# Optimization experiments

Measured on AMD Instinct MI355X. Metric: run time of the kernel, lower is better.

The kernel has to match this reference:

```python
import jax, jax.numpy as jnp
import numpy as np

B, S, D = 4, 2048, 2048
H, HD = 16, 128
ROPE_THETA = 10000.0


def rotate_half(x):
    half = x.shape[-1] // 2
    return jnp.concatenate([-x[..., half:], x[..., :half]], axis=-1)


def setup_inputs() -> dict:
    key = jax.random.key(0)
    ks = jax.random.split(key, 5)
    scale = 1.0 / np.sqrt(D)
    x = jax.random.normal(ks[0], (B, S, D), dtype=jnp.float32)
    wq = jax.random.normal(ks[1], (D, H * HD), dtype=jnp.float32) * scale
    wk = jax.random.normal(ks[2], (D, H * HD), dtype=jnp.float32) * scale
    wv = jax.random.normal(ks[3], (D, H * HD), dtype=jnp.float32) * scale
    wo = jax.random.normal(ks[4], (H * HD, D), dtype=jnp.float32) * scale
    # RoPE frequencies: freqs_cis real/imag parts, shape [S, HD//2]
    inv_freq = 1.0 / (ROPE_THETA ** (np.arange(0, HD, 2, dtype=np.float32) / HD))
    t = np.arange(S, dtype=np.float32)
    freqs = np.outer(t, inv_freq)  # [S, HD//2]
    cos = jnp.asarray(np.cos(freqs), dtype=jnp.float32)
    sin = jnp.asarray(np.sin(freqs), dtype=jnp.float32)
    return {"x": x, "wq": wq, "wk": wk, "wv": wv, "wo": wo, "cos": cos, "sin": sin}


def reference(x, wq, wk, wv, wo, cos, sin):
    batch, seq_len, _ = x.shape
    # QKV projections (no bias), reshape to [b, h, s, d]
    q = (x @ wq).reshape(batch, seq_len, H, HD).transpose(0, 2, 1, 3)
    k = (x @ wk).reshape(batch, seq_len, H, HD).transpose(0, 2, 1, 3)
    v = (x @ wv).reshape(batch, seq_len, H, HD)  # [b, s, h, d]
    # RoPE (half-split / rotate_half convention)
    cos_full = jnp.concatenate([cos, cos], axis=-1)[None, None, :seq_len, :]
    sin_full = jnp.concatenate([sin, sin], axis=-1)[None, None, :seq_len, :]
    q = q * cos_full + rotate_half(q) * sin_full
    k = k * cos_full + rotate_half(k) * sin_full
    # Scaled dot-product attention with causal mask
    logits = jnp.einsum('bhqd,bhkd->bhqk', q, k) / jnp.sqrt(jnp.float32(HD))
    causal = jnp.tril(jnp.ones((seq_len, seq_len), dtype=bool))
    logits = jnp.where(causal[None, None, :, :], logits, -1e10)
    weights = jax.nn.softmax(logits, axis=-1)
    out = jnp.einsum('bhqk,bkhd->bqhd', weights, v)
    out = out.reshape(batch, seq_len, H * HD)
    return out @ wo
```

## Files before the change

kernel.cpp:

```cpp
#include <hip/hip_runtime.h>
#include <cstdint>
#include <cstddef>

typedef unsigned short u16;
using bf16x8  = __attribute__((ext_vector_type(8))) short;
using floatx4 = __attribute__((ext_vector_type(4))) float;

__device__ __forceinline__ u16 f2bf(float f) {
    union { float f; unsigned u; } v; v.f = f;
    unsigned r = v.u + 0x7fffu + ((v.u >> 16) & 1u);
    return (u16)(r >> 16);
}
__device__ __forceinline__ float bf2f(u16 h) {
    union { unsigned u; float f; } v; v.u = ((unsigned)h) << 16; return v.f;
}
__device__ __forceinline__ floatx4 mfma16(bf16x8 a, bf16x8 b, floatx4 c) {
    return __builtin_amdgcn_mfma_f32_16x16x32_bf16(a, b, c, 0, 0, 0);
}
using gptr_t = const __attribute__((address_space(1))) unsigned int*;
using lptr_t = __attribute__((address_space(3))) unsigned int*;
__device__ __forceinline__ void lds16(const void* g, void* l) {
    __builtin_amdgcn_global_load_lds((gptr_t)g, (lptr_t)l, 16, 0, 0);
}
typedef __attribute__((address_space(3))) const u16* lds_cp;
__device__ __forceinline__ bf16x8 dsr128(const u16* p) {
    bf16x8 r;
    asm volatile("ds_read_b128 %0, %1" : "=v"(r) : "v"((lds_cp)p));
    return r;
}

#define ATT_SCALE 0.1275758218522532f

__global__ __launch_bounds__(256) void cvt_x(const float* __restrict__ x, u16* __restrict__ xb) {
    size_t i = ((size_t)blockIdx.x * 256 + threadIdx.x) * 4;
    float4 v = *(const float4*)&x[i];
    ushort4 r; r.x = f2bf(v.x); r.y = f2bf(v.y); r.z = f2bf(v.z); r.w = f2bf(v.w);
    *(ushort4*)&xb[i] = r;
}

__global__ __launch_bounds__(256) void transpose_wall(const float* __restrict__ wq, const float* __restrict__ wk,
                                                      const float* __restrict__ wv, const float* __restrict__ wo,
                                                      u16* __restrict__ wqkvb, u16* __restrict__ wob) {
    __shared__ float t[64][65];
    const int z = blockIdx.z;
    const float* in = (z == 0) ? wq : (z == 1) ? wk : (z == 2) ? wv : wo;
    u16* out = (z < 3) ? (wqkvb + (size_t)z * 2048 * 2048) : wob;
    int k0 = blockIdx.x * 64, n0 = blockIdx.y * 64;
    int tx = threadIdx.x, ty = threadIdx.y;
#pragma unroll
    for (int i = 0; i < 16; ++i) {
        int r = i * 4 + ty;
        t[r][tx] = in[(size_t)(k0 + r) * 2048 + n0 + tx];
    }
    __syncthreads();
#pragma unroll
    for (int i = 0; i < 16; ++i) {
        int r = i * 4 + ty;
        out[(size_t)(n0 + r) * 2048 + k0 + tx] = f2bf(t[tx][r]);
    }
}

template <int MODE>
__global__ __launch_bounds__(512, 2) void gemm_bt(const u16* __restrict__ A, const u16* __restrict__ B,
                                                  u16* __restrict__ Qo, u16* __restrict__ Ko, u16* __restrict__ Vt,
                                                  float* __restrict__ Co) {
    __shared__ __align__(16) u16 sA[2][16384];
    __shared__ __align__(16) u16 sB[2][16384];

    const int nbx = (MODE == 0) ? 24 : 8;
    const int bid = blockIdx.x;
    const int q8 = (int)gridDim.x >> 3;
    const int wg = (bid & 7) * q8 + (bid >> 3);
    const int bx = wg % nbx, by = wg / nbx;
    const int m0 = by << 8, n0 = bx << 8;

    const int tid = threadIdx.x;
    const int w = tid >> 6, lane = tid & 63;
    const int wm = w >> 2, wn = w & 3;
    const int m16 = lane & 15, q4 = lane >> 4;
    const int lr = lane >> 3;
    const int lc8 = (lane & 7) ^ lr;

    const u16* Ag = A + (size_t)(m0 + w * 16 + lr) * 2048 + lc8 * 8;
    const u16* Bg = B + (size_t)(n0 + w * 16 + lr) * 2048 + lc8 * 8;

    const int swz0 = ((q4 ^ (m16 & 7)) << 3);
    const int swz1 = (((4 + q4) ^ (m16 & 7)) << 3);

    floatx4 acc[8][4];
#pragma unroll
    for (int r = 0; r < 8; ++r)
#pragma unroll
        for (int c = 0; c < 4; ++c) acc[r][c] = (floatx4)0.0f;
    bf16x8 af[4][2];
    bf16x8 bf[4][2];

#define STAGE_A(b, h, t) do { \
    lds16(Ag + (size_t)((h) * 128) * 2048 + (t) * 64,     &sA[b][(h) * 8192 + w * 1024]);       \
    lds16(Ag + (size_t)((h) * 128 + 8) * 2048 + (t) * 64, &sA[b][(h) * 8192 + w * 1024 + 512]); \
} while (0)
#define STAGE_B(b, h, t) do { \
    lds16(Bg + (size_t)((h) * 128) * 2048 + (t) * 64,     &sB[b][(h) * 8192 + w * 1024]);       \
    lds16(Bg + (size_t)((h) * 128 + 8) * 2048 + (t) * 64, &sB[b][(h) * 8192 + w * 1024 + 512]); \
} while (0)
#define BAR() __builtin_amdgcn_s_barrier()
#define WAITL0() do { asm volatile("s_waitcnt lgkmcnt(0)" ::: "memory"); __builtin_amdgcn_sched_barrier(0); } while (0)
#define WAITL8() asm volatile("s_waitcnt lgkmcnt(8)" ::: "memory")
#define LDA_(cur, mq) do { _Pragma("unroll") for (int fr = 0; fr < 4; ++fr) { \
    const u16* p = &sA[cur][(wm * 128 + (mq) * 64 + fr * 16 + m16) * 64];      \
    af[fr][0] = dsr128(&p[swz0]);                                              \
    af[fr][1] = dsr128(&p[swz1]); } } while (0)
#define LDB_(cur, nq) do { _Pragma("unroll") for (int c = 0; c < 2; ++c) {     \
    const u16* p = &sB[cur][(wn * 64 + ((nq) * 2 + c) * 16 + m16) * 64];       \
    bf[(nq) * 2 + c][0] = dsr128(&p[swz0]);                                    \
    bf[(nq) * 2 + c][1] = dsr128(&p[swz1]); } } while (0)
#define MM_(mq, nq) do { _Pragma("unroll") for (int kk = 0; kk < 2; ++kk)      \
    _Pragma("unroll") for (int fr = 0; fr < 4; ++fr)                           \
    _Pragma("unroll") for (int c = 0; c < 2; ++c)                              \
        acc[(mq) * 4 + fr][(nq) * 2 + c] =                                     \
            mfma16(af[fr][kk], bf[(nq) * 2 + c][kk], acc[(mq) * 4 + fr][(nq) * 2 + c]); } while (0)

    const int NT = 32;

    STAGE_B(0, 0, 0); STAGE_B(0, 1, 0);
    STAGE_A(0, 0, 0); STAGE_A(0, 1, 0);
    STAGE_B(1, 0, 1); STAGE_B(1, 1, 1);
    asm volatile("s_waitcnt vmcnt(4)" ::: "memory");
    __builtin_amdgcn_s_barrier();

#pragma unroll 2
    for (int t = 0; t < NT; ++t) {
        const int cur = t & 1;
        LDB_(cur, 0);
        LDA_(cur, 0);
        if (t + 1 < NT) STAGE_A(cur ^ 1, 0, t + 1);
        WAITL8();
        BAR();
        WAITL0();
        __builtin_amdgcn_s_setprio(1); MM_(0, 0); __builtin_amdgcn_s_setprio(0);
        BAR();
        LDB_(cur, 1);
        if (t + 1 < NT) STAGE_A(cur ^ 1, 1, t + 1);
        BAR();
        WAITL0();
        __builtin_amdgcn_s_setprio(1); MM_(0, 1); __builtin_amdgcn_s_setprio(0);
        BAR();
        LDA_(cur, 1);
        if (t + 2 < NT) STAGE_B(cur, 0, t + 2);
        BAR();
        WAITL0();
        __builtin_amdgcn_s_setprio(1); MM_(1, 1); __builtin_amdgcn_s_setprio(0);
        BAR();
        if (t + 2 < NT) STAGE_B(cur, 1, t + 2);
        BAR();
        __builtin_amdgcn_s_setprio(1); MM_(1, 0); __builtin_amdgcn_s_setprio(0);
        if (t + 2 < NT)      { asm volatile("s_waitcnt vmcnt(4)" ::: "memory"); }
        else if (t + 1 < NT) { asm volatile("s_waitcnt vmcnt(0)" ::: "memory"); }
        BAR();
    }

#undef STAGE_A
#undef STAGE_B
#undef BAR
#undef WAITL0
#undef WAITL8
#undef LDA_
#undef LDB_
#undef MM_

    if (MODE == 0) {
        const int which = n0 >> 11;
        if (which < 2) {
            u16* dst = (which == 0) ? Qo : Ko;
#pragma unroll
            for (int fr = 0; fr < 8; ++fr) {
                const int mb = m0 + wm * 128 + fr * 16 + q4 * 4;
#pragma unroll
                for (int c = 0; c < 4; ++c) {
                    const int n = n0 + wn * 64 + c * 16 + m16;
                    const int h = (n >> 7) & 15, d = n & 127;
#pragma unroll
                    for (int i = 0; i < 4; ++i) {
                        const int mm = mb + i;
                        const int b = mm >> 11, s = mm & 2047;
                        dst[((size_t)((b * 16 + h) * 2048 + s) << 7) + d] = f2bf(acc[fr][c][i]);
                    }
                }
            }
        } else {
#pragma unroll
            for (int fr = 0; fr < 8; ++fr) {
                const int mb = m0 + wm * 128 + fr * 16 + q4 * 4;
                const int b = mb >> 11, s = mb & 2047;
#pragma unroll
                for (int c = 0; c < 4; ++c) {
                    const int n = n0 + wn * 64 + c * 16 + m16;
                    const int h = (n >> 7) & 15, d = n & 127;
                    ushort4 pk;
                    pk.x = f2bf(acc[fr][c][0]); pk.y = f2bf(acc[fr][c][1]);
                    pk.z = f2bf(acc[fr][c][2]); pk.w = f2bf(acc[fr][c][3]);
                    *(ushort4*)&Vt[((size_t)((b * 16 + h) * 128 + d)) * 2048 + s] = pk;
                }
            }
        }
    } else {
#pragma unroll
        for (int fr = 0; fr < 8; ++fr) {
            const int mb = m0 + wm * 128 + fr * 16 + q4 * 4;
#pragma unroll
            for (int c = 0; c < 4; ++c) {
                const int n = n0 + wn * 64 + c * 16 + m16;
#pragma unroll
                for (int i = 0; i < 4; ++i)
                    Co[(size_t)(mb + i) * 2048 + n] = acc[fr][c][i];
            }
        }
    }
}

__global__ __launch_bounds__(256) void rope_qk(u16* __restrict__ Q, u16* __restrict__ K,
                                               const float* __restrict__ cosb, const float* __restrict__ sinb) {
    int t = blockIdx.x * 256 + threadIdx.x;
    int d4 = (t & 15) * 4;
    int row = t >> 4;
    int s = row & 2047;
    float4 cs = *(const float4*)&cosb[s * 64 + d4];
    float4 sn = *(const float4*)&sinb[s * 64 + d4];
    size_t base = (size_t)row * 128;
    ushort4 qlo = *(ushort4*)&Q[base + d4];
    ushort4 qhi = *(ushort4*)&Q[base + 64 + d4];
    ushort4 klo = *(ushort4*)&K[base + d4];
    ushort4 khi = *(ushort4*)&K[base + 64 + d4];
    float ql[4] = {bf2f(qlo.x), bf2f(qlo.y), bf2f(qlo.z), bf2f(qlo.w)};
    float qh[4] = {bf2f(qhi.x), bf2f(qhi.y), bf2f(qhi.z), bf2f(qhi.w)};
    float kl[4] = {bf2f(klo.x), bf2f(klo.y), bf2f(klo.z), bf2f(klo.w)};
    float kh[4] = {bf2f(khi.x), bf2f(khi.y), bf2f(khi.z), bf2f(khi.w)};
    float c[4] = {cs.x, cs.y, cs.z, cs.w};
    float n[4] = {sn.x, sn.y, sn.z, sn.w};
    ushort4 o0, o1, o2, o3;
    u16* p0 = &o0.x; u16* p1 = &o1.x; u16* p2 = &o2.x; u16* p3 = &o3.x;
#pragma unroll
    for (int i = 0; i < 4; ++i) {
        p0[i] = f2bf((ql[i] * c[i] - qh[i] * n[i]) * ATT_SCALE);
        p1[i] = f2bf((qh[i] * c[i] + ql[i] * n[i]) * ATT_SCALE);
        p2[i] = f2bf(kl[i] * c[i] - kh[i] * n[i]);
        p3[i] = f2bf(kh[i] * c[i] + kl[i] * n[i]);
    }
    *(ushort4*)&Q[base + d4]      = o0;
    *(ushort4*)&Q[base + 64 + d4] = o1;
    *(ushort4*)&K[base + d4]      = o2;
    *(ushort4*)&K[base + 64 + d4] = o3;
}

__global__ __launch_bounds__(512) void attn_kernel(const u16* __restrict__ Q, const u16* __restrict__ K,
                                                   const u16* __restrict__ VT, u16* __restrict__ AO) {
    __shared__ __align__(16) u16 ks[64 * 136];
    __shared__ __align__(16) u16 vts[128 * 72];
    __shared__ __align__(16) u16 ps[256 * 72];
    static const int iqmap[8] = {7, 6, 5, 4, 0, 1, 2, 3};
    const int bx = blockIdx.x;
    const int iq = iqmap[bx >> 6];
    const int bh = bx & 63;
    const int b = bh >> 4, h = bh & 15;
    const u16* Qg = Q  + (size_t)bh * (2048 * 128);
    const u16* Kg = K  + (size_t)bh * (2048 * 128);
    const u16* Vg = VT + (size_t)bh * (128 * 2048);
    const int tid = threadIdx.x, w = tid >> 6, lane = tid & 63;
    const int m16 = lane & 15, q4 = lane >> 4;
    const int jn = 4 * iq + 4;

    const int qrow = iq * 256 + w * 32;
    bf16x8 qf[2][4];
#pragma unroll
    for (int rm = 0; rm < 2; ++rm)
#pragma unroll
        for (int kk = 0; kk < 4; ++kk)
            qf[rm][kk] = *(const bf16x8*)&Qg[(size_t)(qrow + rm * 16 + m16) * 128 + kk * 32 + q4 * 8];

    floatx4 o[2][8];
#pragma unroll
    for (int rm = 0; rm < 2; ++rm)
#pragma unroll
        for (int c = 0; c < 8; ++c) o[rm][c] = (floatx4)0.0f;
    float mrow[2] = {-1e30f, -1e30f}, lrow[2] = {0.0f, 0.0f};

    const int kr0 = tid >> 4,          kc0 = tid & 15;
    const int kr1 = (512 + tid) >> 4,  kc1 = tid & 15;
    const int vr0 = tid >> 3,          vc0 = tid & 7;
    const int vr1 = (512 + tid) >> 3,  vc1 = tid & 7;
    uint4 kreg0, kreg1, vreg0, vreg1;

#define LOADKV(j) do { \
    kreg0 = *(const uint4*)&Kg[(size_t)((j) * 64 + kr0) * 128 + kc0 * 8]; \
    kreg1 = *(const uint4*)&Kg[(size_t)((j) * 64 + kr1) * 128 + kc1 * 8]; \
    vreg0 = *(const uint4*)&Vg[(size_t)vr0 * 2048 + (j) * 64 + vc0 * 8];  \
    vreg1 = *(const uint4*)&Vg[(size_t)vr1 * 2048 + (j) * 64 + vc1 * 8];  \
} while (0)

    LOADKV(0);

    for (int j = 0; j < jn; ++j) {
        asm volatile("" ::: "memory");
        __builtin_amdgcn_s_barrier();
        asm volatile("" ::: "memory");
        *(uint4*)&ks[kr0 * 136 + kc0 * 8] = kreg0;
        *(uint4*)&ks[kr1 * 136 + kc1 * 8] = kreg1;
        *(uint4*)&vts[vr0 * 72 + vc0 * 8] = vreg0;
        *(uint4*)&vts[vr1 * 72 + vc1 * 8] = vreg1;
        if (j + 1 < jn) LOADKV(j + 1);
        asm volatile("s_waitcnt lgkmcnt(0)" ::: "memory");
        __builtin_amdgcn_s_barrier();
        asm volatile("" ::: "memory");

        floatx4 sacc[2][4];
#pragma unroll
        for (int rm = 0; rm < 2; ++rm)
#pragma unroll
            for (int r = 0; r < 4; ++r) sacc[rm][r] = (floatx4)0.0f;
        __builtin_amdgcn_s_setprio(1);
#pragma unroll
        for (int kk = 0; kk < 4; ++kk) {
            bf16x8 kb[4];
#pragma unroll
            for (int r = 0; r < 4; ++r)
                kb[r] = *(const bf16x8*)&ks[(r * 16 + m16) * 136 + kk * 32 + q4 * 8];
#pragma unroll
            for (int rm = 0; rm < 2; ++rm)
#pragma unroll
                for (int r = 0; r < 4; ++r)
                    sacc[rm][r] = mfma16(kb[r], qf[rm][kk], sacc[rm][r]);
        }
        __builtin_amdgcn_s_setprio(0);

        if (j >= 4 * iq) {
#pragma unroll
            for (int rm = 0; rm < 2; ++rm) {
                const int qg = qrow + rm * 16 + m16;
#pragma unroll
                for (int r = 0; r < 4; ++r)
#pragma unroll
                    for (int i = 0; i < 4; ++i) {
                        int kg = j * 64 + r * 16 + q4 * 4 + i;
                        if (kg > qg) sacc[rm][r][i] = -1e30f;
                    }
            }
        }

#pragma unroll
        for (int rm = 0; rm < 2; ++rm) {
            float pmax = -1e30f;
#pragma unroll
            for (int r = 0; r < 4; ++r)
#pragma unroll
                for (int i = 0; i < 4; ++i) pmax = fmaxf(pmax, sacc[rm][r][i]);
            pmax = fmaxf(pmax, __shfl_xor(pmax, 16));
            pmax = fmaxf(pmax, __shfl_xor(pmax, 32));
            float mnew = fmaxf(mrow[rm], pmax);
            float alpha = __builtin_amdgcn_exp2f(mrow[rm] - mnew);
            mrow[rm] = mnew;

            float psum = 0.0f;
#pragma unroll
            for (int r = 0; r < 4; ++r) {
                float p0 = __builtin_amdgcn_exp2f(sacc[rm][r][0] - mnew);
                float p1 = __builtin_amdgcn_exp2f(sacc[rm][r][1] - mnew);
                float p2 = __builtin_amdgcn_exp2f(sacc[rm][r][2] - mnew);
                float p3 = __builtin_amdgcn_exp2f(sacc[rm][r][3] - mnew);
                psum += (p0 + p1) + (p2 + p3);
                ushort4 pk; pk.x = f2bf(p0); pk.y = f2bf(p1); pk.z = f2bf(p2); pk.w = f2bf(p3);
                *(ushort4*)&ps[(w * 32 + rm * 16 + m16) * 72 + r * 16 + q4 * 4] = pk;
            }
            psum += __shfl_xor(psum, 16);
            psum += __shfl_xor(psum, 32);
            lrow[rm] = lrow[rm] * alpha + psum;

            float abc[4];
#pragma unroll
            for (int i = 0; i < 4; ++i) abc[i] = __shfl(alpha, q4 * 4 + i);
#pragma unroll
            for (int c = 0; c < 8; ++c)
#pragma unroll
                for (int i = 0; i < 4; ++i) o[rm][c][i] *= abc[i];
        }

#pragma unroll
        for (int kk = 0; kk < 2; ++kk) {
            bf16x8 pa[2];
#pragma unroll
            for (int rm = 0; rm < 2; ++rm)
                pa[rm] = *(const bf16x8*)&ps[(w * 32 + rm * 16 + m16) * 72 + kk * 32 + q4 * 8];
            __builtin_amdgcn_s_setprio(1);
#pragma unroll
            for (int ch = 0; ch < 2; ++ch) {
                bf16x8 vb[4];
#pragma unroll
                for (int c = 0; c < 4; ++c)
                    vb[c] = *(const bf16x8*)&vts[((ch * 4 + c) * 16 + m16) * 72 + kk * 32 + q4 * 8];
#pragma unroll
                for (int rm = 0; rm < 2; ++rm)
#pragma unroll
                    for (int c = 0; c < 4; ++c)
                        o[rm][ch * 4 + c] = mfma16(pa[rm], vb[c], o[rm][ch * 4 + c]);
            }
            __builtin_amdgcn_s_setprio(0);
        }
    }
#undef LOADKV

#pragma unroll
    for (int rm = 0; rm < 2; ++rm) {
        float linv = __builtin_amdgcn_rcpf(lrow[rm]);
        float li[4];
#pragma unroll
        for (int i = 0; i < 4; ++i) li[i] = __shfl(linv, q4 * 4 + i);
#pragma unroll
        for (int c = 0; c < 8; ++c)
#pragma unroll
            for (int i = 0; i < 4; ++i) {
                int s = qrow + rm * 16 + q4 * 4 + i;
                int d = c * 16 + m16;
                AO[((size_t)(b * 2048 + s)) * 2048 + h * 128 + d] = f2bf(o[rm][c][i] * li[i]);
            }
    }
}

extern "C" void kernel_launch(void* const* d_in, const int* in_sizes, int n_in,
                              void* d_out, int out_size, void* d_ws, size_t ws_size,
                              hipStream_t stream) {
    const float* x    = (const float*)d_in[0];
    const float* wq   = (const float*)d_in[1];
    const float* wk   = (const float*)d_in[2];
    const float* wv   = (const float*)d_in[3];
    const float* wo   = (const float*)d_in[4];
    const float* cosb = (const float*)d_in[5];
    const float* sinb = (const float*)d_in[6];
    float* out = (float*)d_out;

    char* ws = (char*)d_ws;
    u16* xb    = (u16*)(ws);
    u16* AO    = xb;
    u16* wqkvb = (u16*)(ws + 33554432);
    u16* wob   = (u16*)(ws + 58720256);
    u16* Qb    = (u16*)(ws + 67108864);
    u16* Kb    = (u16*)(ws + 100663296);
    u16* Vtb   = (u16*)(ws + 134217728);

    cvt_x<<<16384, 256, 0, stream>>>(x, xb);
    transpose_wall<<<dim3(32, 32, 4), dim3(64, 4), 0, stream>>>(wq, wk, wv, wo, wqkvb, wob);

    gemm_bt<0><<<768, 512, 0, stream>>>(xb, wqkvb, Qb, Kb, Vtb, nullptr);
    rope_qk<<<8192, 256, 0, stream>>>(Qb, Kb, cosb, sinb);
    attn_kernel<<<512, 512, 0, stream>>>(Qb, Kb, Vtb, AO);
    gemm_bt<1><<<256, 512, 0, stream>>>(AO, wob, nullptr, nullptr, nullptr, out);
}
```

Baseline: 564.1 us.

## Fuse RoPE into QKV GEMM epilogue by remapping wave column ownership

Removes the separate RoPE kernel and applies the rotation and attention scale inside the QKV projection GEMM epilogue. The per-wave N-column mapping is changed so each wave holds both the low and high half-dimensions of a head, which lets it rotate values from registers. This avoids a full extra read and write pass over Q and K in global memory, plus one kernel launch. In exchange, the epilogue does scattered cos/sin loads and carries a little more address arithmetic.

```diff
diff --git a/kernel.cpp b/kernel.cpp
--- a/kernel.cpp
+++ b/kernel.cpp
@@ -63,7 +63,8 @@
 template <int MODE>
 __global__ __launch_bounds__(512, 2) void gemm_bt(const u16* __restrict__ A, const u16* __restrict__ B,
                                                   u16* __restrict__ Qo, u16* __restrict__ Ko, u16* __restrict__ Vt,
-                                                  float* __restrict__ Co) {
+                                                  float* __restrict__ Co,
+                                                  const float* __restrict__ cosb, const float* __restrict__ sinb) {
     __shared__ __align__(16) u16 sA[2][16384];
     __shared__ __align__(16) u16 sB[2][16384];
 
@@ -80,6 +81,7 @@
     const int m16 = lane & 15, q4 = lane >> 4;
     const int lr = lane >> 3;
     const int lc8 = (lane & 7) ^ lr;
+    const int wnbase = (wn >> 1) * 128 + (wn & 1) * 32;
 
     const u16* Ag = A + (size_t)(m0 + w * 16 + lr) * 2048 + lc8 * 8;
     const u16* Bg = B + (size_t)(n0 + w * 16 + lr) * 2048 + lc8 * 8;
@@ -111,9 +113,10 @@
     af[fr][0] = dsr128(&p[swz0]);                                              \
     af[fr][1] = dsr128(&p[swz1]); } } while (0)
 #define LDB_(cur, nq) do { _Pragma("unroll") for (int c = 0; c < 2; ++c) {     \
-    const u16* p = &sB[cur][(wn * 64 + ((nq) * 2 + c) * 16 + m16) * 64];       \
-    bf[(nq) * 2 + c][0] = dsr128(&p[swz0]);                                    \
-    bf[(nq) * 2 + c][1] = dsr128(&p[swz1]); } } while (0)
+    const int j = (nq) * 2 + c;                                                \
+    const u16* p = &sB[cur][(wnbase + (j & 1) * 16 + (j >> 1) * 64 + m16) * 64]; \
+    bf[j][0] = dsr128(&p[swz0]);                                               \
+    bf[j][1] = dsr128(&p[swz1]); } } while (0)
 #define MM_(mq, nq) do { _Pragma("unroll") for (int kk = 0; kk < 2; ++kk)      \
     _Pragma("unroll") for (int fr = 0; fr < 4; ++fr)                           \
     _Pragma("unroll") for (int c = 0; c < 2; ++c)                              \
@@ -172,18 +175,25 @@
         const int which = n0 >> 11;
         if (which < 2) {
             u16* dst = (which == 0) ? Qo : Ko;
+            const float sc = (which == 0) ? ATT_SCALE : 1.0f;
+            const int h = ((n0 >> 7) + (wn >> 1)) & 15;
+            const int dp0 = (wn & 1) * 32 + m16;
 #pragma unroll
             for (int fr = 0; fr < 8; ++fr) {
                 const int mb = m0 + wm * 128 + fr * 16 + q4 * 4;
 #pragma unroll
-                for (int c = 0; c < 4; ++c) {
-                    const int n = n0 + wn * 64 + c * 16 + m16;
-                    const int h = (n >> 7) & 15, d = n & 127;
+                for (int c0 = 0; c0 < 2; ++c0) {
+                    const int dp = dp0 + c0 * 16;
 #pragma unroll
                     for (int i = 0; i < 4; ++i) {
                         const int mm = mb + i;
                         const int b = mm >> 11, s = mm & 2047;
-                        dst[((size_t)((b * 16 + h) * 2048 + s) << 7) + d] = f2bf(acc[fr][c][i]);
+                        const float cs = cosb[(size_t)s * 64 + dp];
+                        const float sn = sinb[(size_t)s * 64 + dp];
+                        const float lo = acc[fr][c0][i], hi = acc[fr][c0 + 2][i];
+                        const size_t base = ((size_t)((b * 16 + h) * 2048 + s) << 7) + dp;
+                        dst[base]      = f2bf((lo * cs - hi * sn) * sc);
+                        dst[base + 64] = f2bf((hi * cs + lo * sn) * sc);
                     }
                 }
             }
@@ -194,7 +204,7 @@
                 const int b = mb >> 11, s = mb & 2047;
 #pragma unroll
                 for (int c = 0; c < 4; ++c) {
-                    const int n = n0 + wn * 64 + c * 16 + m16;
+                    const int n = n0 + wnbase + (c & 1) * 16 + (c >> 1) * 64 + m16;
                     const int h = (n >> 7) & 15, d = n & 127;
                     ushort4 pk;
                     pk.x = f2bf(acc[fr][c][0]); pk.y = f2bf(acc[fr][c][1]);
@@ -209,47 +219,13 @@
             const int mb = m0 + wm * 128 + fr * 16 + q4 * 4;
 #pragma unroll
             for (int c = 0; c < 4; ++c) {
-                const int n = n0 + wn * 64 + c * 16 + m16;
+                const int n = n0 + wnbase + (c & 1) * 16 + (c >> 1) * 64 + m16;
 #pragma unroll
                 for (int i = 0; i < 4; ++i)
                     Co[(size_t)(mb + i) * 2048 + n] = acc[fr][c][i];
             }
         }
     }
-}
-
-__global__ __launch_bounds__(256) void rope_qk(u16* __restrict__ Q, u16* __restrict__ K,
-                                               const float* __restrict__ cosb, const float* __restrict__ sinb) {
-    int t = blockIdx.x * 256 + threadIdx.x;
-    int d4 = (t & 15) * 4;
-    int row = t >> 4;
-    int s = row & 2047;
-    float4 cs = *(const float4*)&cosb[s * 64 + d4];
-    float4 sn = *(const float4*)&sinb[s * 64 + d4];
-    size_t base = (size_t)row * 128;
-    ushort4 qlo = *(ushort4*)&Q[base + d4];
-    ushort4 qhi = *(ushort4*)&Q[base + 64 + d4];
-    ushort4 klo = *(ushort4*)&K[base + d4];
-    ushort4 khi = *(ushort4*)&K[base + 64 + d4];
-    float ql[4] = {bf2f(qlo.x), bf2f(qlo.y), bf2f(qlo.z), bf2f(qlo.w)};
-    float qh[4] = {bf2f(qhi.x), bf2f(qhi.y), bf2f(qhi.z), bf2f(qhi.w)};
-    float kl[4] = {bf2f(klo.x), bf2f(klo.y), bf2f(klo.z), bf2f(klo.w)};
-    float kh[4] = {bf2f(khi.x), bf2f(khi.y), bf2f(khi.z), bf2f(khi.w)};
-    float c[4] = {cs.x, cs.y, cs.z, cs.w};
-    float n[4] = {sn.x, sn.y, sn.z, sn.w};
-    ushort4 o0, o1, o2, o3;
-    u16* p0 = &o0.x; u16* p1 = &o1.x; u16* p2 = &o2.x; u16* p3 = &o3.x;
-#pragma unroll
-    for (int i = 0; i < 4; ++i) {
-        p0[i] = f2bf((ql[i] * c[i] - qh[i] * n[i]) * ATT_SCALE);
-        p1[i] = f2bf((qh[i] * c[i] + ql[i] * n[i]) * ATT_SCALE);
-        p2[i] = f2bf(kl[i] * c[i] - kh[i] * n[i]);
-        p3[i] = f2bf(kh[i] * c[i] + kl[i] * n[i]);
-    }
-    *(ushort4*)&Q[base + d4]      = o0;
-    *(ushort4*)&Q[base + 64 + d4] = o1;
-    *(ushort4*)&K[base + d4]      = o2;
-    *(ushort4*)&K[base + 64 + d4] = o3;
 }
 
 __global__ __launch_bounds__(512) void attn_kernel(const u16* __restrict__ Q, const u16* __restrict__ K,
@@ -448,8 +424,7 @@
     cvt_x<<<16384, 256, 0, stream>>>(x, xb);
     transpose_wall<<<dim3(32, 32, 4), dim3(64, 4), 0, stream>>>(wq, wk, wv, wo, wqkvb, wob);
 
-    gemm_bt<0><<<768, 512, 0, stream>>>(xb, wqkvb, Qb, Kb, Vtb, nullptr);
-    rope_qk<<<8192, 256, 0, stream>>>(Qb, Kb, cosb, sinb);
+    gemm_bt<0><<<768, 512, 0, stream>>>(xb, wqkvb, Qb, Kb, Vtb, nullptr, cosb, sinb);
     attn_kernel<<<512, 512, 0, stream>>>(Qb, Kb, Vtb, AO);
-    gemm_bt<1><<<256, 512, 0, stream>>>(AO, wob, nullptr, nullptr, nullptr, out);
-}
+    gemm_bt<1><<<256, 512, 0, stream>>>(AO, wob, nullptr, nullptr, nullptr, out, nullptr, nullptr);
+}
```

New measurement: 548.2 us. -2.8%, faster.
